# Optimization experiments

Hardware: AMD Instinct MI355X
Metric: run time of the kernel (lower is better)

The kernel has to match this reference:

```python
import jax, jax.numpy as jnp
import numpy as np

N_WIRES = 4
DIM = 16  # 2**N_WIRES

# PauliZ eigenvalue signs per wire per basis state (wire 0 = MSB, torchquantum convention)
_Z = np.array([[1.0 - 2.0 * ((i >> (N_WIRES - 1 - w)) & 1) for i in range(DIM)]
               for w in range(N_WIRES)], dtype=np.float32)  # [4,16]

def _cnot_perm(c, t):
    mc = 1 << (N_WIRES - 1 - c)
    mt = 1 << (N_WIRES - 1 - t)
    return np.array([i ^ mt if (i & mc) else i for i in range(DIM)])

_PERM_WRAP = [_cnot_perm(0, 1), _cnot_perm(1, 2), _cnot_perm(2, 3), _cnot_perm(3, 0)]  # QLSTM ladder
_PERM_LINE = [_cnot_perm(0, 1), _cnot_perm(1, 2), _cnot_perm(2, 3)]                   # kernel ladder

def _apply_rx(state, theta, wire):
    """Apply RX(theta) on `wire`. state: [B,16] complex64. theta: scalar or [B]."""
    theta = jnp.asarray(theta)
    c = jnp.cos(theta / 2).astype(jnp.complex64)
    s = jnp.sin(theta / 2).astype(jnp.complex64)
    left = 2 ** wire
    right = 2 ** (N_WIRES - 1 - wire)
    st = state.reshape(-1, left, 2, right)
    a, b = st[:, :, 0, :], st[:, :, 1, :]
    if theta.ndim != 0:
        c = c[:, None, None]
        s = s[:, None, None]
    na = c * a - 1j * s * b
    nb = -1j * s * a + c * b
    return jnp.stack([na, nb], axis=2).reshape(-1, DIM)

def _circuit(angles, params, perms):
    """angles: [B,4] encoding RX angles; params: [4] trainable RX angles."""
    B = angles.shape[0]
    state = jnp.zeros((B, DIM), jnp.complex64).at[:, 0].set(1.0)
    for w in range(N_WIRES):
        state = _apply_rx(state, angles[:, w], w)
    for w in range(N_WIRES):
        state = _apply_rx(state, params[w], w)
    for p in perms:
        state = state[:, p]
    return state

def _measure_z(state):
    probs = state.real ** 2 + state.imag ** 2  # [B,16]
    return probs @ jnp.asarray(_Z).T           # [B,4]

def setup_inputs() -> dict:
    key = jax.random.key(0)
    ks = jax.random.split(key, 16)
    T, B, D, S, H = 128, 64, 32, 1024, 4
    inp = {
        'x': jax.random.normal(ks[0], (T, B, D), jnp.float32),
        'support_vectors': jax.random.normal(ks[1], (S, D), jnp.float32),
        'Wf': jax.random.normal(ks[2], (H, D + H), jnp.float32) * 0.1,
        'bf': jax.random.normal(ks[3], (H,), jnp.float32) * 0.1,
        'Wi': jax.random.normal(ks[4], (H, D + H), jnp.float32) * 0.1,
        'bi': jax.random.normal(ks[5], (H,), jnp.float32) * 0.1,
        'Wu': jax.random.normal(ks[6], (H, D + H), jnp.float32) * 0.1,
        'bu': jax.random.normal(ks[7], (H,), jnp.float32) * 0.1,
        'Wo': jax.random.normal(ks[8], (H, D + H), jnp.float32) * 0.1,
        'bo': jax.random.normal(ks[9], (H,), jnp.float32) * 0.1,
        'pf': jax.random.normal(ks[10], (H,), jnp.float32),
        'pi': jax.random.normal(ks[11], (H,), jnp.float32),
        'pu': jax.random.normal(ks[12], (H,), jnp.float32),
        'po': jax.random.normal(ks[13], (H,), jnp.float32),
        'qk_params': jax.random.normal(ks[14], (H,), jnp.float32),
    }
    return inp

def reference(x, support_vectors, Wf, bf, Wi, bi, Wu, bu, Wo, bo, pf, pi, pu, po, qk_params):
    T, B, D = x.shape
    gamma = 1.0
    xf = x.reshape(T * B, D)

    # classical RBF Gram matrix (materializes [N,S,D] diff, as in the original)
    diff = xf[:, None, :] - support_vectors[None, :, :]
    rbf = jnp.exp(-gamma * jnp.sum(diff * diff, axis=-1))  # [N,S]

    # quantum kernel: encode first 4 features, trainable RX, linear CNOT ladder
    sx = _circuit(xf[:, :4], qk_params, _PERM_LINE)               # [N,16] complex
    sy = _circuit(support_vectors[:, :4], qk_params, _PERM_LINE)  # [S,16] complex
    qk = jnp.abs(sx @ sy.T)  # no conjugation, matching torch.matmul(states_x, states_y.t())

    def gate(comb, W, b, p):
        return _measure_z(_circuit(comb @ W.T + b, p, _PERM_WRAP))

    def step(carry, xt):
        hx, cx = carry
        comb = jnp.concatenate([xt, hx], axis=1)
        f = jax.nn.sigmoid(gate(comb, Wf, bf, pf))
        i = jax.nn.sigmoid(gate(comb, Wi, bi, pi))
        g = jnp.tanh(gate(comb, Wu, bu, pu))
        o = jax.nn.sigmoid(gate(comb, Wo, bo, po))
        cx = f * cx + i * g
        hx = o * jnp.tanh(cx)
        return (hx, cx), hx

    h0 = jnp.zeros((B, N_WIRES), jnp.float32)
    c0 = jnp.zeros((B, N_WIRES), jnp.float32)
    (_, _), outs = jax.lax.scan(step, (h0, c0), x)  # outs: [T,B,4]
    return (outs, rbf, qk)
```

## Files before the change

### kernel.cpp

```cpp
#include <hip/hip_runtime.h>

#define T_STEPS 128
#define BATCH   64
#define DIMX    32
#define S_SUP   1024
#define NROW    8192
#define OUT_H_SZ   (T_STEPS*BATCH*4)
#define OUT_RBF_SZ (NROW*S_SUP)

__device__ __forceinline__ float rcp_fast(float x) { return __builtin_amdgcn_rcpf(x); }

template<int K>
__device__ __forceinline__ float quad_bcast(float v) {
    constexpr int ctrl = K * 0x55;
    return __builtin_bit_cast(float,
        __builtin_amdgcn_mov_dpp(__builtin_bit_cast(int, v), ctrl, 0xF, 0xF, true));
}

__global__ __launch_bounds__(256) void pre_kernel(
    const float* __restrict__ x,
    const float* __restrict__ Wf, const float* __restrict__ bf,
    const float* __restrict__ Wi, const float* __restrict__ bi,
    const float* __restrict__ Wu, const float* __restrict__ bu,
    const float* __restrict__ Wo, const float* __restrict__ bo,
    const float* __restrict__ pf, const float* __restrict__ pi,
    const float* __restrict__ pu, const float* __restrict__ po,
    float* __restrict__ pre)
{
    const int tid = threadIdx.x;
    const int rl  = tid >> 4;
    const int gw  = tid & 15;
    const int g   = gw >> 2, w = gw & 3;
    const int row = blockIdx.x * 16 + rl;

    __shared__ float xs[16 * DIMX];
    if (tid < 128) {
        ((float4*)xs)[tid] = ((const float4*)(x + (size_t)blockIdx.x * 16 * DIMX))[tid];
    }
    __syncthreads();

    const float* W  = (g == 0) ? Wf : (g == 1) ? Wi : (g == 2) ? Wu : Wo;
    const float* bb = (g == 0) ? bf : (g == 1) ? bi : (g == 2) ? bu : bo;
    const float* pp = (g == 0) ? pf : (g == 1) ? pi : (g == 2) ? pu : po;

    float acc = bb[w] + pp[w];
    const float* Wr = W + w * 36;
    const float* xr = xs + rl * DIMX;
#pragma unroll
    for (int d = 0; d < DIMX; d++) acc += xr[d] * Wr[d];

    pre[(row * 4 + g) * 4 + w] = acc;
}

__global__ __launch_bounds__(256) void fused_kernel(
    const float* __restrict__ x,  const float* __restrict__ sv,
    const float* __restrict__ Wf, const float* __restrict__ bf,
    const float* __restrict__ Wi, const float* __restrict__ bi,
    const float* __restrict__ Wu, const float* __restrict__ bu,
    const float* __restrict__ Wo, const float* __restrict__ bo,
    const float* __restrict__ pf, const float* __restrict__ pi,
    const float* __restrict__ pu, const float* __restrict__ po,
    const float* __restrict__ qkp, const float* __restrict__ pre,
    float* __restrict__ out_h, float* __restrict__ out_rbf, float* __restrict__ out_qk)
{
    __shared__ float xs[BATCH * DIMX];
    __shared__ float xn2[BATCH];
    const int tid = threadIdx.x;

    if (blockIdx.x == 0) {
        __builtin_amdgcn_s_setprio(3);
        const int b = tid >> 2, g = tid & 3;
        const float* W = (g == 0) ? Wf : (g == 1) ? Wi : (g == 2) ? Wu : Wo;

        float Wh[4][4];
#pragma unroll
        for (int w = 0; w < 4; w++)
#pragma unroll
            for (int j = 0; j < 4; j++) Wh[w][j] = W[w * 36 + 32 + j];

        const float kexp = (g == 2) ? -2.f : -1.f;
        const float Aa   = (g == 2) ?  2.f :  1.f;
        const float Bb   = (g == 2) ? -1.f :  0.f;
        const bool  isg1 = (g == 1), isg2 = (g == 2), isg3 = (g == 3);

        float h0 = 0.f, h1 = 0.f, h2 = 0.f, h3 = 0.f;
        float c0 = 0.f, c1 = 0.f, c2 = 0.f, c3 = 0.f;
        const int base = b * 4 + g;
        const float4* prep = (const float4*)pre;

        auto lstm_step = [&](int t, float4 cur) {
            float a0 = cur.x, a1 = cur.y, a2 = cur.z, a3 = cur.w;
            a0 += h0 * Wh[0][0] + h1 * Wh[0][1] + h2 * Wh[0][2] + h3 * Wh[0][3];
            a1 += h0 * Wh[1][0] + h1 * Wh[1][1] + h2 * Wh[1][2] + h3 * Wh[1][3];
            a2 += h0 * Wh[2][0] + h1 * Wh[2][1] + h2 * Wh[2][2] + h3 * Wh[2][3];
            a3 += h0 * Wh[3][0] + h1 * Wh[3][1] + h2 * Wh[3][2] + h3 * Wh[3][3];

            float C0 = __cosf(a0), C1 = __cosf(a1), C2 = __cosf(a2), C3 = __cosf(a3);
            float t23 = C2 * C3;
            float m01 = C0 * C1;
            float r0 = C1 * t23;
            float r1 = m01;
            float r2 = m01 * C2;
            float r3 = m01 * t23;

            float o0 = Aa * rcp_fast(1.f + __expf(r0 * kexp)) + Bb;
            float o1 = Aa * rcp_fast(1.f + __expf(r1 * kexp)) + Bb;
            float o2 = Aa * rcp_fast(1.f + __expf(r2 * kexp)) + Bb;
            float o3 = Aa * rcp_fast(1.f + __expf(r3 * kexp)) + Bb;

            float f0 = quad_bcast<0>(o0), f1 = quad_bcast<0>(o1), f2 = quad_bcast<0>(o2), f3 = quad_bcast<0>(o3);
            float i0 = quad_bcast<1>(o0), i1 = quad_bcast<1>(o1), i2 = quad_bcast<1>(o2), i3 = quad_bcast<1>(o3);
            float u0 = quad_bcast<2>(o0), u1 = quad_bcast<2>(o1), u2 = quad_bcast<2>(o2), u3 = quad_bcast<2>(o3);
            float z0 = quad_bcast<3>(o0), z1 = quad_bcast<3>(o1), z2 = quad_bcast<3>(o2), z3 = quad_bcast<3>(o3);

            c0 = f0 * c0 + i0 * u0;
            c1 = f1 * c1 + i1 * u1;
            c2 = f2 * c2 + i2 * u2;
            c3 = f3 * c3 + i3 * u3;

            float t0 = 2.f * rcp_fast(1.f + __expf(-2.f * c0)) - 1.f;
            float t1 = 2.f * rcp_fast(1.f + __expf(-2.f * c1)) - 1.f;
            float t2 = 2.f * rcp_fast(1.f + __expf(-2.f * c2)) - 1.f;
            float t3 = 2.f * rcp_fast(1.f + __expf(-2.f * c3)) - 1.f;
            h0 = z0 * t0; h1 = z1 * t1; h2 = z2 * t2; h3 = z3 * t3;

            float hsel = isg1 ? h1 : h0;
            hsel = isg2 ? h2 : hsel;
            hsel = isg3 ? h3 : hsel;
            out_h[t * 256 + tid] = hsel;
        };

        float4 cb0, cb1, cb2, cb3, cb4, cb5, cb6, cb7;
        cb0 = prep[base];           cb1 = prep[base + 256];
        cb2 = prep[base + 512];     cb3 = prep[base + 768];
        cb4 = prep[base + 1024];    cb5 = prep[base + 1280];
        cb6 = prep[base + 1536];    cb7 = prep[base + 1792];

#pragma unroll 1
        for (int tt = 0; tt < T_STEPS; tt += 8) {
            int nb = tt + 8; nb = (nb > T_STEPS - 8) ? (T_STEPS - 8) : nb;
            const float4* pc = prep + base + nb * 256;
            float4 nb0 = pc[0];
            float4 nb1 = pc[256];
            float4 nb2 = pc[512];
            float4 nb3 = pc[768];
            float4 nb4 = pc[1024];
            float4 nb5 = pc[1280];
            float4 nb6 = pc[1536];
            float4 nb7 = pc[1792];
            __builtin_amdgcn_sched_barrier(0);

            lstm_step(tt + 0, cb0);
            lstm_step(tt + 1, cb1);
            lstm_step(tt + 2, cb2);
            lstm_step(tt + 3, cb3);
            lstm_step(tt + 4, cb4);
            lstm_step(tt + 5, cb5);
            lstm_step(tt + 6, cb6);
            lstm_step(tt + 7, cb7);

            cb0 = nb0; cb1 = nb1; cb2 = nb2; cb3 = nb3;
            cb4 = nb4; cb5 = nb5; cb6 = nb6; cb7 = nb7;
        }
    } else {
        const int bid = blockIdx.x - 1;
        const int n0  = (bid >> 2) * BATCH;
        const int s0  = (bid & 3) * 256;

        float4* xs4 = (float4*)xs;
        const float4* xg = (const float4*)(x + (size_t)n0 * DIMX);
        float4 t0v = xg[tid];
        float4 t1v = xg[tid + 256];
        xs4[tid]       = t0v;
        xs4[tid + 256] = t1v;

        float p0 = t0v.x * t0v.x + t0v.y * t0v.y + t0v.z * t0v.z + t0v.w * t0v.w;
        float p1 = t1v.x * t1v.x + t1v.y * t1v.y + t1v.z * t1v.z + t1v.w * t1v.w;
        p0 += __shfl_xor(p0, 1); p1 += __shfl_xor(p1, 1);
        p0 += __shfl_xor(p0, 2); p1 += __shfl_xor(p1, 2);
        p0 += __shfl_xor(p0, 4); p1 += __shfl_xor(p1, 4);
        if ((tid & 7) == 0) {
            xn2[tid >> 3]        = p0;
            xn2[(tid >> 3) + 32] = p1;
        }

        const int s = s0 + tid;
        float4 svv[8];
        const float4* svg = (const float4*)(sv + (size_t)s * DIMX);
#pragma unroll
        for (int k = 0; k < 8; k++) svv[k] = svg[k];
        float sn2 = 0.f;
#pragma unroll
        for (int k = 0; k < 8; k++)
            sn2 += svv[k].x * svv[k].x + svv[k].y * svv[k].y + svv[k].z * svv[k].z + svv[k].w * svv[k].w;

        const float B0 = 0.5f * svv[0].x + qkp[0];
        const float B1 = 0.5f * svv[0].y + qkp[1];
        const float B2 = 0.5f * svv[0].z + qkp[2];
        const float B3 = 0.5f * svv[0].w + qkp[3];
        __syncthreads();

#pragma unroll 4
        for (int n = 0; n < BATCH; n++) {
            const float4* xr4 = (const float4*)(xs + n * DIMX);
            float4 xv0 = xr4[0];
            float dot = xv0.x * svv[0].x + xv0.y * svv[0].y + xv0.z * svv[0].z + xv0.w * svv[0].w;
#pragma unroll
            for (int k = 1; k < 8; k++) {
                float4 xv = xr4[k];
                dot += xv.x * svv[k].x + xv.y * svv[k].y + xv.z * svv[k].z + xv.w * svv[k].w;
            }
            float dist = xn2[n] + sn2 - 2.f * dot;
            float rb   = __expf(-dist);

            float qv = __cosf(0.5f * xv0.x + B0) * __cosf(0.5f * xv0.y + B1)
                     * __cosf(0.5f * xv0.z + B2) * __cosf(0.5f * xv0.w + B3);
            qv = fabsf(qv);

            const int row = n0 + n;
            out_rbf[(size_t)row * S_SUP + s] = rb;
            out_qk [(size_t)row * S_SUP + s] = qv;
        }
    }
}

extern "C" void kernel_launch(void* const* d_in, const int* in_sizes, int n_in,
                              void* d_out, int out_size, void* d_ws, size_t ws_size,
                              hipStream_t stream)
{
    const float* x   = (const float*)d_in[0];
    const float* sv  = (const float*)d_in[1];
    const float* Wf  = (const float*)d_in[2];
    const float* bf  = (const float*)d_in[3];
    const float* Wi  = (const float*)d_in[4];
    const float* bi  = (const float*)d_in[5];
    const float* Wu  = (const float*)d_in[6];
    const float* bu  = (const float*)d_in[7];
    const float* Wo  = (const float*)d_in[8];
    const float* bo  = (const float*)d_in[9];
    const float* pf  = (const float*)d_in[10];
    const float* pi  = (const float*)d_in[11];
    const float* pu  = (const float*)d_in[12];
    const float* po  = (const float*)d_in[13];
    const float* qkp = (const float*)d_in[14];

    float* out     = (float*)d_out;
    float* out_h   = out;
    float* out_rbf = out + OUT_H_SZ;
    float* out_qk  = out + OUT_H_SZ + OUT_RBF_SZ;

    float* pre = (float*)d_ws;

    pre_kernel<<<NROW / 16, 256, 0, stream>>>(x, Wf, bf, Wi, bi, Wu, bu, Wo, bo,
                                              pf, pi, pu, po, pre);
    fused_kernel<<<1 + 512, 256, 0, stream>>>(
        x, sv, Wf, bf, Wi, bi, Wu, bu, Wo, bo, pf, pi, pu, po, qkp, pre,
        out_h, out_rbf, out_qk);
}
```

Baseline: 152.0 us.

## Retile RBF/qk blocks to 512 threads, use native exp2/cos and Pade tanh

Blocks now cover 32 rows by all 1024 support vectors, with each thread handling two support vectors. Each LDS x-row read therefore serves two dot products, and the grid is halved to 257 blocks of 512 threads. Transcendentals switch to the hardware exp2 and revolution-based cos intrinsics, with the 1/2pi and log2e scaling folded into the precomputed terms. The LSTM tanh becomes a Pade rational approximation, and the recurrent block uses only 32 lanes per wave. The Pade tanh loses accuracy for large cell values, and the two-vector register tiling raises register pressure.

```diff
diff --git a/kernel.cpp b/kernel.cpp
--- a/kernel.cpp
+++ b/kernel.cpp
@@ -8,13 +8,25 @@
 #define OUT_H_SZ   (T_STEPS*BATCH*4)
 #define OUT_RBF_SZ (NROW*S_SUP)
 
-__device__ __forceinline__ float rcp_fast(float x) { return __builtin_amdgcn_rcpf(x); }
+#define INV2PI 0.15915494309189535f
+#define L2E    1.4426950408889634f
+
+__device__ __forceinline__ float rcp_fast(float x)  { return __builtin_amdgcn_rcpf(x); }
+__device__ __forceinline__ float exp2_fast(float x) { return __builtin_amdgcn_exp2f(x); }
+__device__ __forceinline__ float cos_rev(float x)   { return __builtin_amdgcn_cosf(x); }
 
 template<int K>
 __device__ __forceinline__ float quad_bcast(float v) {
     constexpr int ctrl = K * 0x55;
     return __builtin_bit_cast(float,
         __builtin_amdgcn_mov_dpp(__builtin_bit_cast(int, v), ctrl, 0xF, 0xF, true));
+}
+
+__device__ __forceinline__ float tanh_pade(float x) {
+    float q = x * x;
+    float n = x * fmaf(q, q + 105.f, 945.f);
+    float d = fmaf(q, fmaf(q, 15.f, 420.f), 945.f);
+    return n * rcp_fast(d);
 }
 
 __global__ __launch_bounds__(256) void pre_kernel(
@@ -49,10 +61,10 @@
 #pragma unroll
     for (int d = 0; d < DIMX; d++) acc += xr[d] * Wr[d];
 
-    pre[(row * 4 + g) * 4 + w] = acc;
-}
-
-__global__ __launch_bounds__(256) void fused_kernel(
+    pre[(row * 4 + g) * 4 + w] = acc * INV2PI;
+}
+
+__global__ __launch_bounds__(512, 2) void fused_kernel(
     const float* __restrict__ x,  const float* __restrict__ sv,
     const float* __restrict__ Wf, const float* __restrict__ bf,
     const float* __restrict__ Wi, const float* __restrict__ bi,
@@ -63,24 +75,28 @@
     const float* __restrict__ qkp, const float* __restrict__ pre,
     float* __restrict__ out_h, float* __restrict__ out_rbf, float* __restrict__ out_qk)
 {
-    __shared__ float xs[BATCH * DIMX];
-    __shared__ float xn2[BATCH];
+    __shared__ float xs[32 * DIMX];
+    __shared__ float xn2[32];
     const int tid = threadIdx.x;
 
     if (blockIdx.x == 0) {
         __builtin_amdgcn_s_setprio(3);
-        const int b = tid >> 2, g = tid & 3;
+        const int lane = tid & 63;
+        if (lane >= 32) return;
+        const int wv = tid >> 6;
+        const int b  = wv * 8 + (lane >> 2);
+        const int g  = lane & 3;
         const float* W = (g == 0) ? Wf : (g == 1) ? Wi : (g == 2) ? Wu : Wo;
 
         float Wh[4][4];
 #pragma unroll
         for (int w = 0; w < 4; w++)
 #pragma unroll
-            for (int j = 0; j < 4; j++) Wh[w][j] = W[w * 36 + 32 + j];
-
-        const float kexp = (g == 2) ? -2.f : -1.f;
-        const float Aa   = (g == 2) ?  2.f :  1.f;
-        const float Bb   = (g == 2) ? -1.f :  0.f;
+            for (int j = 0; j < 4; j++) Wh[w][j] = W[w * 36 + 32 + j] * INV2PI;
+
+        const float K2 = (g == 2) ? (-2.f * L2E) : (-L2E);
+        const float Aa = (g == 2) ?  2.f :  1.f;
+        const float Bb = (g == 2) ? -1.f :  0.f;
         const bool  isg1 = (g == 1), isg2 = (g == 2), isg3 = (g == 3);
 
         float h0 = 0.f, h1 = 0.f, h2 = 0.f, h3 = 0.f;
@@ -95,7 +111,7 @@
             a2 += h0 * Wh[2][0] + h1 * Wh[2][1] + h2 * Wh[2][2] + h3 * Wh[2][3];
             a3 += h0 * Wh[3][0] + h1 * Wh[3][1] + h2 * Wh[3][2] + h3 * Wh[3][3];
 
-            float C0 = __cosf(a0), C1 = __cosf(a1), C2 = __cosf(a2), C3 = __cosf(a3);
+            float C0 = cos_rev(a0), C1 = cos_rev(a1), C2 = cos_rev(a2), C3 = cos_rev(a3);
             float t23 = C2 * C3;
             float m01 = C0 * C1;
             float r0 = C1 * t23;
@@ -103,10 +119,10 @@
             float r2 = m01 * C2;
             float r3 = m01 * t23;
 
-            float o0 = Aa * rcp_fast(1.f + __expf(r0 * kexp)) + Bb;
-            float o1 = Aa * rcp_fast(1.f + __expf(r1 * kexp)) + Bb;
-            float o2 = Aa * rcp_fast(1.f + __expf(r2 * kexp)) + Bb;
-            float o3 = Aa * rcp_fast(1.f + __expf(r3 * kexp)) + Bb;
+            float o0 = fmaf(Aa, rcp_fast(1.f + exp2_fast(r0 * K2)), Bb);
+            float o1 = fmaf(Aa, rcp_fast(1.f + exp2_fast(r1 * K2)), Bb);
+            float o2 = fmaf(Aa, rcp_fast(1.f + exp2_fast(r2 * K2)), Bb);
+            float o3 = fmaf(Aa, rcp_fast(1.f + exp2_fast(r3 * K2)), Bb);
 
             float f0 = quad_bcast<0>(o0), f1 = quad_bcast<0>(o1), f2 = quad_bcast<0>(o2), f3 = quad_bcast<0>(o3);
             float i0 = quad_bcast<1>(o0), i1 = quad_bcast<1>(o1), i2 = quad_bcast<1>(o2), i3 = quad_bcast<1>(o3);
@@ -118,16 +134,16 @@
             c2 = f2 * c2 + i2 * u2;
             c3 = f3 * c3 + i3 * u3;
 
-            float t0 = 2.f * rcp_fast(1.f + __expf(-2.f * c0)) - 1.f;
-            float t1 = 2.f * rcp_fast(1.f + __expf(-2.f * c1)) - 1.f;
-            float t2 = 2.f * rcp_fast(1.f + __expf(-2.f * c2)) - 1.f;
-            float t3 = 2.f * rcp_fast(1.f + __expf(-2.f * c3)) - 1.f;
+            float t0 = tanh_pade(c0);
+            float t1 = tanh_pade(c1);
+            float t2 = tanh_pade(c2);
+            float t3 = tanh_pade(c3);
             h0 = z0 * t0; h1 = z1 * t1; h2 = z2 * t2; h3 = z3 * t3;
 
             float hsel = isg1 ? h1 : h0;
             hsel = isg2 ? h2 : hsel;
             hsel = isg3 ? h3 : hsel;
-            out_h[t * 256 + tid] = hsel;
+            out_h[t * 256 + base] = hsel;
         };
 
         float4 cb0, cb1, cb2, cb3, cb4, cb5, cb6, cb7;
@@ -164,62 +180,75 @@
         }
     } else {
         const int bid = blockIdx.x - 1;
-        const int n0  = (bid >> 2) * BATCH;
-        const int s0  = (bid & 3) * 256;
+        const int n0  = bid * 32;
 
         float4* xs4 = (float4*)xs;
         const float4* xg = (const float4*)(x + (size_t)n0 * DIMX);
-        float4 t0v = xg[tid];
-        float4 t1v = xg[tid + 256];
-        xs4[tid]       = t0v;
-        xs4[tid + 256] = t1v;
-
-        float p0 = t0v.x * t0v.x + t0v.y * t0v.y + t0v.z * t0v.z + t0v.w * t0v.w;
-        float p1 = t1v.x * t1v.x + t1v.y * t1v.y + t1v.z * t1v.z + t1v.w * t1v.w;
-        p0 += __shfl_xor(p0, 1); p1 += __shfl_xor(p1, 1);
-        p0 += __shfl_xor(p0, 2); p1 += __shfl_xor(p1, 2);
-        p0 += __shfl_xor(p0, 4); p1 += __shfl_xor(p1, 4);
-        if ((tid & 7) == 0) {
-            xn2[tid >> 3]        = p0;
-            xn2[(tid >> 3) + 32] = p1;
-        }
-
-        const int s = s0 + tid;
-        float4 svv[8];
-        const float4* svg = (const float4*)(sv + (size_t)s * DIMX);
-#pragma unroll
-        for (int k = 0; k < 8; k++) svv[k] = svg[k];
-        float sn2 = 0.f;
-#pragma unroll
-        for (int k = 0; k < 8; k++)
-            sn2 += svv[k].x * svv[k].x + svv[k].y * svv[k].y + svv[k].z * svv[k].z + svv[k].w * svv[k].w;
-
-        const float B0 = 0.5f * svv[0].x + qkp[0];
-        const float B1 = 0.5f * svv[0].y + qkp[1];
-        const float B2 = 0.5f * svv[0].z + qkp[2];
-        const float B3 = 0.5f * svv[0].w + qkp[3];
+        if (tid < 256) {
+            float4 t0v = xg[tid];
+            xs4[tid] = t0v;
+            float p0 = t0v.x * t0v.x + t0v.y * t0v.y + t0v.z * t0v.z + t0v.w * t0v.w;
+            p0 += __shfl_xor(p0, 1);
+            p0 += __shfl_xor(p0, 2);
+            p0 += __shfl_xor(p0, 4);
+            if ((tid & 7) == 0) xn2[tid >> 3] = -L2E * p0;
+        }
+
+        const int sA = tid, sB = tid + 512;
+        float4 svv[8], svw[8];
+        const float4* svgA = (const float4*)(sv + (size_t)sA * DIMX);
+        const float4* svgB = (const float4*)(sv + (size_t)sB * DIMX);
+#pragma unroll
+        for (int k = 0; k < 8; k++) { svv[k] = svgA[k]; svw[k] = svgB[k]; }
+        float sn2A = 0.f, sn2B = 0.f;
+#pragma unroll
+        for (int k = 0; k < 8; k++) {
+            sn2A += svv[k].x * svv[k].x + svv[k].y * svv[k].y + svv[k].z * svv[k].z + svv[k].w * svv[k].w;
+            sn2B += svw[k].x * svw[k].x + svw[k].y * svw[k].y + svw[k].z * svw[k].z + svw[k].w * svw[k].w;
+        }
+        const float snlA = -L2E * sn2A;
+        const float snlB = -L2E * sn2B;
+
+        const float q0 = qkp[0], q1 = qkp[1], q2 = qkp[2], q3 = qkp[3];
+        const float C05 = 0.5f * INV2PI;
+        const float BA0 = fmaf(0.5f, svv[0].x, q0) * INV2PI;
+        const float BA1 = fmaf(0.5f, svv[0].y, q1) * INV2PI;
+        const float BA2 = fmaf(0.5f, svv[0].z, q2) * INV2PI;
+        const float BA3 = fmaf(0.5f, svv[0].w, q3) * INV2PI;
+        const float BB0 = fmaf(0.5f, svw[0].x, q0) * INV2PI;
+        const float BB1 = fmaf(0.5f, svw[0].y, q1) * INV2PI;
+        const float BB2 = fmaf(0.5f, svw[0].z, q2) * INV2PI;
+        const float BB3 = fmaf(0.5f, svw[0].w, q3) * INV2PI;
         __syncthreads();
 
-#pragma unroll 4
-        for (int n = 0; n < BATCH; n++) {
+#pragma unroll 2
+        for (int n = 0; n < 32; n++) {
             const float4* xr4 = (const float4*)(xs + n * DIMX);
             float4 xv0 = xr4[0];
-            float dot = xv0.x * svv[0].x + xv0.y * svv[0].y + xv0.z * svv[0].z + xv0.w * svv[0].w;
+            float dotA = xv0.x * svv[0].x + xv0.y * svv[0].y + xv0.z * svv[0].z + xv0.w * svv[0].w;
+            float dotB = xv0.x * svw[0].x + xv0.y * svw[0].y + xv0.z * svw[0].z + xv0.w * svw[0].w;
 #pragma unroll
             for (int k = 1; k < 8; k++) {
                 float4 xv = xr4[k];
-                dot += xv.x * svv[k].x + xv.y * svv[k].y + xv.z * svv[k].z + xv.w * svv[k].w;
+                dotA += xv.x * svv[k].x + xv.y * svv[k].y + xv.z * svv[k].z + xv.w * svv[k].w;
+                dotB += xv.x * svw[k].x + xv.y * svw[k].y + xv.z * svw[k].z + xv.w * svw[k].w;
             }
-            float dist = xn2[n] + sn2 - 2.f * dot;
-            float rb   = __expf(-dist);
-
-            float qv = __cosf(0.5f * xv0.x + B0) * __cosf(0.5f * xv0.y + B1)
-                     * __cosf(0.5f * xv0.z + B2) * __cosf(0.5f * xv0.w + B3);
-            qv = fabsf(qv);
-
-            const int row = n0 + n;
-            out_rbf[(size_t)row * S_SUP + s] = rb;
-            out_qk [(size_t)row * S_SUP + s] = qv;
+            float xnl = xn2[n];
+            float rbA = exp2_fast(fmaf(2.f * L2E, dotA, xnl + snlA));
+            float rbB = exp2_fast(fmaf(2.f * L2E, dotB, xnl + snlB));
+
+            float qvA = cos_rev(fmaf(C05, xv0.x, BA0)) * cos_rev(fmaf(C05, xv0.y, BA1))
+                      * cos_rev(fmaf(C05, xv0.z, BA2)) * cos_rev(fmaf(C05, xv0.w, BA3));
+            float qvB = cos_rev(fmaf(C05, xv0.x, BB0)) * cos_rev(fmaf(C05, xv0.y, BB1))
+                      * cos_rev(fmaf(C05, xv0.z, BB2)) * cos_rev(fmaf(C05, xv0.w, BB3));
+            qvA = fabsf(qvA);
+            qvB = fabsf(qvB);
+
+            const size_t rowb = (size_t)(n0 + n) * S_SUP;
+            out_rbf[rowb + sA] = rbA;
+            out_rbf[rowb + sB] = rbB;
+            out_qk [rowb + sA] = qvA;
+            out_qk [rowb + sB] = qvB;
         }
     }
 }
@@ -253,7 +282,7 @@
 
     pre_kernel<<<NROW / 16, 256, 0, stream>>>(x, Wf, bf, Wi, bi, Wu, bu, Wo, bo,
                                               pf, pi, pu, po, pre);
-    fused_kernel<<<1 + 512, 256, 0, stream>>>(
+    fused_kernel<<<1 + 256, 512, 0, stream>>>(
         x, sv, Wf, bf, Wi, bi, Wu, bu, Wo, bo, pf, pi, pu, po, qkp, pre,
         out_h, out_rbf, out_qk);
 }
```

After: 166.0 us. +9.2%, slower.
